# Performance work log

Hardware: AMD Instinct MI355X
Metric: run time of the kernel (lower is better)

The kernel has to match this reference:

```python
import jax, jax.numpy as jnp
import numpy as np

HIDDEN = 768
FFN = 3072
E = 8
TOP_K = 2


def setup_inputs() -> dict:
    key = jax.random.key(0)
    k_x, k_r, k_w1, k_w2 = jax.random.split(key, 4)
    x = jax.random.normal(k_x, (1, 1024, HIDDEN), dtype=jnp.float32)
    # nn.Linear(hidden, E, bias=False): weight applied as x @ W^T; store as [H, E]
    bound = 1.0 / np.sqrt(HIDDEN)
    router_w = jax.random.uniform(k_r, (HIDDEN, E), minval=-bound, maxval=bound, dtype=jnp.float32)
    w1 = jax.random.normal(k_w1, (E, HIDDEN, FFN), dtype=jnp.float32) * 0.02
    w2 = jax.random.normal(k_w2, (E, FFN, HIDDEN), dtype=jnp.float32) * 0.02
    return {"x": x, "router_w": router_w, "w1": w1, "w2": w2}


def reference(x, router_w, w1, w2):
    B, T, H = x.shape
    xf = x.reshape(-1, H)                                  # [N, H]
    logits = xf @ router_w                                 # [N, E] (eval mode: no noise)
    probs = jax.nn.softmax(logits, axis=-1)
    top_v, top_i = jax.lax.top_k(probs, TOP_K)             # [N, K]
    top_v = top_v / jnp.sum(top_v, axis=-1, keepdims=True)  # renormalize top-k probs
    # Combine top-k weights into a dense per-expert gate; zero gates make the
    # dense per-expert computation mathematically identical to sparse dispatch.
    gates = jnp.sum(jax.nn.one_hot(top_i, E, dtype=xf.dtype) * top_v[..., None], axis=1)  # [N, E]
    h = jax.nn.gelu(jnp.einsum('nh,ehf->enf', xf, w1), approximate=False)  # [E, N, F]
    y = jnp.einsum('enf,efh->enh', h, w2)                  # [E, N, H]
    out = jnp.einsum('ne,enh->nh', gates, y)               # [N, H]
    return out.reshape(B, T, H)
```

## Files before the change

kernel.cpp:

```cpp
#include <hip/hip_runtime.h>
#include <cmath>

#define NTOK 1024
#define HD   768
#define FF   3072
#define NE   8
#define NSLOT (NTOK * 2)
#define BK   64

#define NB_ROUTER 256
#define NB_CONV   4608
#define NB_FFN1   1152
#define KSPLIT    4
#define KSEG      (FF / KSPLIT)
#define NB_FFN2   (24 * 6 * KSPLIT)

typedef unsigned short u16;
typedef unsigned int   u32;
typedef __bf16 bf16x8 __attribute__((ext_vector_type(8)));
typedef float  f32x4  __attribute__((ext_vector_type(4)));
typedef u16    u16x8  __attribute__((ext_vector_type(8)));

__device__ __forceinline__ u16 f2bf(float f) {
  union { float f; u32 u; } v; v.f = f;
  u32 r = v.u + 0x7FFFu + ((v.u >> 16) & 1u);
  return (u16)(r >> 16);
}

__device__ __forceinline__ void load16(const void* g, void* l) {
  __builtin_amdgcn_global_load_lds(
      (const __attribute__((address_space(1))) u32*)g,
      (__attribute__((address_space(3))) u32*)l, 16, 0, 0);
}

__device__ __forceinline__ void conv_tile_dma(
    const float* __restrict__ src, u16* __restrict__ dst,
    int K, int N, int k0, int n0, float* lt, int tid, int lane, int wid)
{
  const int kr = wid * 16;
#pragma unroll
  for (int j = 0; j < 4; ++j) {
    const int k  = kr + j * 4 + (lane >> 4);
    const int sc = ((lane & 15) * 4) ^ (((k >> 3) & 3) << 3);
    load16(src + (size_t)(k0 + k) * N + n0 + sc,
           lt + (size_t)(kr + j * 4) * 64);
  }
  __syncthreads();
#pragma unroll
  for (int h = 0; h < 2; ++h) {
    const int c  = tid + h * 256;
    const int n  = c >> 3;
    const int ko = c & 7;
    const int sx = (ko & 3) << 3;
    u16x8 vv;
#pragma unroll
    for (int d = 0; d < 8; ++d)
      vv[d] = f2bf(lt[(ko * 8 + d) * 64 + (n ^ sx)]);
    *(u16x8*)(dst + (size_t)(n0 + n) * K + k0 + ko * 8) = vv;
  }
}

__global__ __launch_bounds__(256) void conv1_router_kernel(
    const float* __restrict__ w1, u16* __restrict__ w1t,
    const float* __restrict__ x, const float* __restrict__ rw,
    u16* __restrict__ xb, int* __restrict__ ti, float* __restrict__ tg,
    int* __restrict__ tos, float* __restrict__ gos, int* __restrict__ seg,
    int* __restrict__ done, float* __restrict__ out)
{
  __shared__ __align__(16) float lt[64 * 64];
  __shared__ int soff[NE], scnt[NE], spos[NE], lastFlag;
  const int tid  = threadIdx.x;
  const int lane = tid & 63;
  const int wid  = tid >> 6;

  if (blockIdx.x >= NB_ROUTER) {
    const int cid = blockIdx.x - NB_ROUTER;
    const int z   = cid / 576;
    const int rem = cid % 576;
    conv_tile_dma(w1 + (size_t)z * HD * FF, w1t + (size_t)z * FF * HD,
                  HD, FF, (rem / 48) * 64, (rem % 48) * 64, lt, tid, lane, wid);
    return;
  }

  {
    float4* o4 = (float4*)out;
    const float4 zz = {0.f, 0.f, 0.f, 0.f};
#pragma unroll
    for (int i = 0; i < 3; ++i) o4[(size_t)blockIdx.x * 768 + i * 256 + tid] = zz;
  }

  const int t = blockIdx.x * 4 + wid;
  const float* xrow = x + (size_t)t * HD;
  u16* xbrow = xb + (size_t)t * HD;

  float acc[NE] = {};
#pragma unroll
  for (int j = 0; j < 12; ++j) {
    const int h = lane + j * 64;
    const float xv = xrow[h];
    xbrow[h] = f2bf(xv);
    const float4 r0 = *(const float4*)(rw + h * 8);
    const float4 r1 = *(const float4*)(rw + h * 8 + 4);
    acc[0] += xv * r0.x; acc[1] += xv * r0.y;
    acc[2] += xv * r0.z; acc[3] += xv * r0.w;
    acc[4] += xv * r1.x; acc[5] += xv * r1.y;
    acc[6] += xv * r1.z; acc[7] += xv * r1.w;
  }
#pragma unroll
  for (int e = 0; e < NE; ++e) {
    float v = acc[e];
#pragma unroll
    for (int off = 32; off; off >>= 1) v += __shfl_down(v, off, 64);
    acc[e] = v;
  }
  if (lane == 0) {
    float v0 = -1e30f, v1 = -1e30f; int i0 = 0, i1 = 0;
#pragma unroll
    for (int e = 0; e < NE; ++e) {
      const float p = acc[e];
      if (p > v0) { v1 = v0; i1 = i0; v0 = p; i0 = e; }
      else if (p > v1) { v1 = p; i1 = e; }
    }
    const float e1 = expf(v1 - v0);
    ti[2 * t] = i0;      ti[2 * t + 1] = i1;
    tg[2 * t] = 1.0f / (1.0f + e1);
    tg[2 * t + 1] = e1 / (1.0f + e1);
  }

  __syncthreads();
  __threadfence();
  if (tid == 0) lastFlag = (atomicAdd(done, 1) == NB_ROUTER - 1);
  __syncthreads();
  if (!lastFlag) return;
  __threadfence();

  if (tid < NE) scnt[tid] = 0;
  __syncthreads();
  int   mye[8]; float myg[8];
#pragma unroll
  for (int j = 0; j < 8; ++j) {
    const int s = tid * 8 + j;
    mye[j] = ti[s]; myg[j] = tg[s];
    atomicAdd(&scnt[mye[j]], 1);
  }
  __syncthreads();
  if (tid == 0) {
    int o = 0;
    for (int e = 0; e < NE; ++e) {
      soff[e] = o; seg[e] = o; seg[NE + e] = scnt[e]; o += scnt[e];
    }
  }
  if (tid < NE) spos[tid] = 0;
  __syncthreads();
#pragma unroll
  for (int j = 0; j < 8; ++j) {
    const int s = tid * 8 + j;
    const int p = atomicAdd(&spos[mye[j]], 1);
    const int o = soff[mye[j]] + p;
    tos[o] = s >> 1;
    gos[o] = myg[j];
  }
}

__device__ __forceinline__ int find_expert(const int* __restrict__ seg,
                                           int mt, int* m0_out) {
  int e = -1, m0 = 0, off = 0;
#pragma unroll
  for (int ee = 0; ee < NE; ++ee) {
    const int T = (seg[NE + ee] + 127) >> 7;
    if (e < 0 && mt < off + T) { e = ee; m0 = (mt - off) << 7; }
    off += T;
  }
  *m0_out = m0;
  return e;
}

__global__ __launch_bounds__(256) void ffn1_conv2_kernel(
    const u16* __restrict__ xb, const u16* __restrict__ w1t,
    const int* __restrict__ tos, const int* __restrict__ seg,
    u16* __restrict__ hbuf,
    const float* __restrict__ w2, u16* __restrict__ w2t)
{
  __shared__ __align__(16) char smem[25088];
  const int tid  = threadIdx.x;
  const int lane = tid & 63;
  const int wid  = tid >> 6;

  const int g  = blockIdx.x / 5;
  const int r5 = blockIdx.x % 5;

  if (r5) {
    const int cid = g * 4 + (r5 - 1);
    const int z   = cid / 576;
    const int rem = cid % 576;
    conv_tile_dma(w2 + (size_t)z * FF * HD, w2t + (size_t)z * HD * FF,
                  FF, HD, (rem % 48) * 64, (rem / 48) * 64,
                  (float*)smem, tid, lane, wid);
    return;
  }

  const int mt = g / 48, nt = g % 48;
  int m0;
  const int e = find_expert(seg, mt, &m0);
  if (e < 0) return;
  const int cnt   = seg[NE + e];
  const int start = seg[e];
  const int n0    = nt * 64;

  u16* As   = (u16*)smem;
  u16* Bs   = (u16*)(smem + 16384);
  int* toks = (int*)(smem + 24576);

  if (tid < 128) toks[tid] = tos[start + min(m0 + tid, cnt - 1)];
  __syncthreads();

  const int rsub = lane >> 3;
  const int c8   = (lane & 7) ^ rsub;

  const u16* ag[4]; u16* al[4];
#pragma unroll
  for (int i = 0; i < 4; ++i) {
    const int rb = wid * 8 + i * 32;
    ag[i] = xb + (size_t)toks[rb + rsub] * HD + c8 * 8;
    al[i] = As + rb * 64;
  }
  const u16* bg[2]; u16* bl[2];
#pragma unroll
  for (int i = 0; i < 2; ++i) {
    const int rb = wid * 8 + i * 32;
    bg[i] = w1t + ((size_t)e * FF + n0 + rb + rsub) * HD + c8 * 8;
    bl[i] = Bs + rb * 64;
  }

  const int wm  = (wid >> 1) << 6;
  const int wn  = (wid & 1) << 5;
  const int q   = lane >> 4;
  const int r16 = lane & 15;

  f32x4 acc[4][2] = {};

  for (int k0 = 0; k0 < HD; k0 += BK) {
#pragma unroll
    for (int i = 0; i < 4; ++i) load16(ag[i] + k0, al[i]);
#pragma unroll
    for (int i = 0; i < 2; ++i) load16(bg[i] + k0, bl[i]);
    __syncthreads();
#pragma unroll
    for (int s = 0; s < 2; ++s) {
      const int pa = ((s << 2) + q) ^ (r16 & 7);
      bf16x8 af[4], bf[2];
#pragma unroll
      for (int t = 0; t < 4; ++t)
        af[t] = *(const bf16x8*)(&As[(wm + t * 16 + r16) * 64 + pa * 8]);
#pragma unroll
      for (int t = 0; t < 2; ++t)
        bf[t] = *(const bf16x8*)(&Bs[(wn + t * 16 + r16) * 64 + pa * 8]);
#pragma unroll
      for (int t = 0; t < 4; ++t)
#pragma unroll
        for (int c = 0; c < 2; ++c)
          acc[t][c] = __builtin_amdgcn_mfma_f32_16x16x32_bf16(af[t], bf[c], acc[t][c], 0, 0, 0);
    }
    __syncthreads();
  }

#pragma unroll
  for (int t = 0; t < 4; ++t) {
    const int mbase = m0 + wm + t * 16 + q * 4;
#pragma unroll
    for (int i = 0; i < 4; ++i) {
      if (mbase + i < cnt) {
        u16* drow = hbuf + (size_t)(start + mbase + i) * FF + n0 + wn;
#pragma unroll
        for (int c = 0; c < 2; ++c) {
          float v = acc[t][c][i];
          v = 0.5f * v * (1.0f + erff(v * 0.70710678118f));
          drow[c * 16 + r16] = f2bf(v);
        }
      }
    }
  }
}

__global__ __launch_bounds__(256) void ffn2_kernel(
    const u16* __restrict__ hbuf, const u16* __restrict__ w2t,
    const int* __restrict__ tos, const float* __restrict__ gos,
    const int* __restrict__ seg, float* __restrict__ out)
{
  const int fid  = blockIdx.x;
  const int mt   = fid / 24;
  const int rest = fid % 24;
  const int n0   = (rest >> 2) << 7;
  const int ks   = rest & 3;
  int m0;
  const int e = find_expert(seg, mt, &m0);
  if (e < 0) return;
  const int cnt   = seg[NE + e];
  const int start = seg[e];
  const int kbase = ks * KSEG;

  __shared__ __align__(16) u16 As[128 * 64];
  __shared__ __align__(16) u16 Bs[128 * 64];
  __shared__ int   toks[128];
  __shared__ float gates[128];

  const int tid = threadIdx.x;
  if (tid < 128) {
    const int idx = start + min(m0 + tid, cnt - 1);
    toks[tid]  = tos[idx];
    gates[tid] = gos[idx];
  }
  __syncthreads();

  const int lane = tid & 63;
  const int wid  = tid >> 6;
  const int rsub = lane >> 3;
  const int c8   = (lane & 7) ^ rsub;

  const u16* ag[4]; u16* al[4];
#pragma unroll
  for (int i = 0; i < 4; ++i) {
    const int rb = wid * 8 + i * 32;
    ag[i] = hbuf + (size_t)(start + min(m0 + rb + rsub, cnt - 1)) * FF + kbase + c8 * 8;
    al[i] = As + rb * 64;
  }
  const u16* bg[4]; u16* bl[4];
#pragma unroll
  for (int i = 0; i < 4; ++i) {
    const int rb = wid * 8 + i * 32;
    bg[i] = w2t + ((size_t)e * HD + n0 + rb + rsub) * FF + kbase + c8 * 8;
    bl[i] = Bs + rb * 64;
  }

  const int wm  = (wid >> 1) << 6;
  const int wn  = (wid & 1) << 6;
  const int q   = lane >> 4;
  const int r16 = lane & 15;

  f32x4 acc[4][4] = {};

  for (int k0 = 0; k0 < KSEG; k0 += BK) {
#pragma unroll
    for (int i = 0; i < 4; ++i) load16(ag[i] + k0, al[i]);
#pragma unroll
    for (int i = 0; i < 4; ++i) load16(bg[i] + k0, bl[i]);
    __syncthreads();
#pragma unroll
    for (int s = 0; s < 2; ++s) {
      const int pa = ((s << 2) + q) ^ (r16 & 7);
      bf16x8 af[4], bf[4];
#pragma unroll
      for (int t = 0; t < 4; ++t)
        af[t] = *(const bf16x8*)(&As[(wm + t * 16 + r16) * 64 + pa * 8]);
#pragma unroll
      for (int c = 0; c < 4; ++c)
        bf[c] = *(const bf16x8*)(&Bs[(wn + c * 16 + r16) * 64 + pa * 8]);
#pragma unroll
      for (int t = 0; t < 4; ++t)
#pragma unroll
        for (int c = 0; c < 4; ++c)
          acc[t][c] = __builtin_amdgcn_mfma_f32_16x16x32_bf16(af[t], bf[c], acc[t][c], 0, 0, 0);
    }
    __syncthreads();
  }

#pragma unroll
  for (int t = 0; t < 4; ++t) {
    const int mbase = wm + t * 16 + q * 4;
#pragma unroll
    for (int i = 0; i < 4; ++i) {
      const int mloc = mbase + i;
      if (m0 + mloc < cnt) {
        const int tok  = toks[mloc];
        const float gv = gates[mloc];
        float* drow = out + (size_t)tok * HD + n0 + wn;
#pragma unroll
        for (int c = 0; c < 4; ++c)
          atomicAdd(drow + c * 16 + r16, gv * acc[t][c][i]);
      }
    }
  }
}

extern "C" void kernel_launch(void* const* d_in, const int* in_sizes, int n_in,
                              void* d_out, int out_size, void* d_ws, size_t ws_size,
                              hipStream_t stream) {
  const float* x  = (const float*)d_in[0];
  const float* rw = (const float*)d_in[1];
  const float* w1 = (const float*)d_in[2];
  const float* w2 = (const float*)d_in[3];
  float* out = (float*)d_out;

  char* ws = (char*)d_ws;
  const size_t o_xb    = 0;
  const size_t o_hbuf  = o_xb + (size_t)NTOK * HD * 2;
  const size_t o_tos   = o_hbuf + (size_t)NSLOT * FF * 2;
  const size_t o_gos   = o_tos + (size_t)NSLOT * 4;
  const size_t o_seg   = o_gos + (size_t)NSLOT * 4;
  const size_t o_done  = o_seg + 64 * 4;
  const size_t o_ti    = o_done + 64;
  const size_t o_tg    = o_ti + (size_t)NSLOT * 4;
  const size_t o_w1t   = (o_tg + (size_t)NSLOT * 4 + 255) & ~(size_t)255;
  const size_t o_w2t   = o_w1t + (size_t)NE * HD * FF * 2;
  u16*   xb    = (u16*)(ws + o_xb);
  u16*   hbuf  = (u16*)(ws + o_hbuf);
  int*   tos   = (int*)(ws + o_tos);
  float* gos   = (float*)(ws + o_gos);
  int*   seg   = (int*)(ws + o_seg);
  int*   done  = (int*)(ws + o_done);
  int*   ti    = (int*)(ws + o_ti);
  float* tg    = (float*)(ws + o_tg);
  u16*   w1t   = (u16*)(ws + o_w1t);
  u16*   w2t   = (u16*)(ws + o_w2t);

  hipMemsetAsync(done, 0, 64, stream);
  hipLaunchKernelGGL(conv1_router_kernel, dim3(NB_ROUTER + NB_CONV), dim3(256), 0, stream,
                     w1, w1t, x, rw, xb, ti, tg, tos, gos, seg, done, out);
  hipLaunchKernelGGL(ffn1_conv2_kernel, dim3(NB_FFN1 * 5), dim3(256), 0, stream,
                     xb, w1t, tos, seg, hbuf, w2, w2t);
  hipLaunchKernelGGL(ffn2_kernel, dim3(NB_FFN2), dim3(256), 0, stream,
                     hbuf, w2t, tos, gos, seg, out);
}
```

Baseline: 273.6 us.

## Fuse MoE pipeline into one persistent kernel with grid barriers

Replaces the three launches (router+w1 conversion, ffn1+w2 conversion, ffn2) with a single 1024-block persistent kernel that separates phases with atomic grid barriers. The weight transpose-convert tiles change to 128x64 tiles that use register loads and a padded LDS transpose instead of LDS DMA. ffn2 tiles are narrowed to 64 columns to produce more work units. The aim is to remove launch gaps and tail effects between stages. It relies on all 1024 blocks being co-resident for the spin barriers, and risks deadlock or stalls if occupancy is insufficient.

```diff
diff --git a/kernel.cpp b/kernel.cpp
--- a/kernel.cpp
+++ b/kernel.cpp
@@ -7,13 +7,20 @@
 #define NE   8
 #define NSLOT (NTOK * 2)
 #define BK   64
-
+#define CLD  130
+
+#define NBLK      1024
 #define NB_ROUTER 256
-#define NB_CONV   4608
-#define NB_FFN1   1152
+
+#define NT_CONV   2304
+#define NU_FFN1   1152
+#define NU_P1     (NU_FFN1 + NT_CONV)
 #define KSPLIT    4
 #define KSEG      (FF / KSPLIT)
-#define NB_FFN2   (24 * 6 * KSPLIT)
+#define NU_FFN2   (24 * 12 * KSPLIT)
+
+#define TGT1 (NBLK + 1)
+#define TGT2 (TGT1 + NBLK)
 
 typedef unsigned short u16;
 typedef unsigned int   u32;
@@ -33,132 +40,36 @@
       (__attribute__((address_space(3))) u32*)l, 16, 0, 0);
 }
 
-__device__ __forceinline__ void conv_tile_dma(
+__device__ __forceinline__ void conv_tile(
     const float* __restrict__ src, u16* __restrict__ dst,
-    int K, int N, int k0, int n0, float* lt, int tid, int lane, int wid)
+    int K, int N, int k0, int n0, u16* lt, int tid, int lane, int wid)
 {
-  const int kr = wid * 16;
-#pragma unroll
-  for (int j = 0; j < 4; ++j) {
-    const int k  = kr + j * 4 + (lane >> 4);
-    const int sc = ((lane & 15) * 4) ^ (((k >> 3) & 3) << 3);
-    load16(src + (size_t)(k0 + k) * N + n0 + sc,
-           lt + (size_t)(kr + j * 4) * 64);
+  const int rr = tid >> 4;
+  const int cc = (tid & 15) << 2;
+
+  const float* s0 = src + (size_t)(k0 + rr) * N + n0 + cc;
+  float4 v[8];
+#pragma unroll
+  for (int j = 0; j < 8; ++j) v[j] = *(const float4*)(s0 + (size_t)j * 16 * N);
+  __builtin_amdgcn_sched_barrier(0);
+
+#pragma unroll
+  for (int j = 0; j < 8; ++j) {
+    const int k = j * 16 + rr;
+    lt[(cc + 0) * CLD + k] = f2bf(v[j].x); lt[(cc + 1) * CLD + k] = f2bf(v[j].y);
+    lt[(cc + 2) * CLD + k] = f2bf(v[j].z); lt[(cc + 3) * CLD + k] = f2bf(v[j].w);
   }
   __syncthreads();
-#pragma unroll
-  for (int h = 0; h < 2; ++h) {
-    const int c  = tid + h * 256;
-    const int n  = c >> 3;
-    const int ko = c & 7;
-    const int sx = (ko & 3) << 3;
+
+  const int l15 = lane & 15;
+  const int r4  = lane >> 4;
+#pragma unroll
+  for (int s = 0; s < 4; ++s) {
+    const int r = wid * 16 + s * 4 + r4;
     u16x8 vv;
 #pragma unroll
-    for (int d = 0; d < 8; ++d)
-      vv[d] = f2bf(lt[(ko * 8 + d) * 64 + (n ^ sx)]);
-    *(u16x8*)(dst + (size_t)(n0 + n) * K + k0 + ko * 8) = vv;
-  }
-}
-
-__global__ __launch_bounds__(256) void conv1_router_kernel(
-    const float* __restrict__ w1, u16* __restrict__ w1t,
-    const float* __restrict__ x, const float* __restrict__ rw,
-    u16* __restrict__ xb, int* __restrict__ ti, float* __restrict__ tg,
-    int* __restrict__ tos, float* __restrict__ gos, int* __restrict__ seg,
-    int* __restrict__ done, float* __restrict__ out)
-{
-  __shared__ __align__(16) float lt[64 * 64];
-  __shared__ int soff[NE], scnt[NE], spos[NE], lastFlag;
-  const int tid  = threadIdx.x;
-  const int lane = tid & 63;
-  const int wid  = tid >> 6;
-
-  if (blockIdx.x >= NB_ROUTER) {
-    const int cid = blockIdx.x - NB_ROUTER;
-    const int z   = cid / 576;
-    const int rem = cid % 576;
-    conv_tile_dma(w1 + (size_t)z * HD * FF, w1t + (size_t)z * FF * HD,
-                  HD, FF, (rem / 48) * 64, (rem % 48) * 64, lt, tid, lane, wid);
-    return;
-  }
-
-  {
-    float4* o4 = (float4*)out;
-    const float4 zz = {0.f, 0.f, 0.f, 0.f};
-#pragma unroll
-    for (int i = 0; i < 3; ++i) o4[(size_t)blockIdx.x * 768 + i * 256 + tid] = zz;
-  }
-
-  const int t = blockIdx.x * 4 + wid;
-  const float* xrow = x + (size_t)t * HD;
-  u16* xbrow = xb + (size_t)t * HD;
-
-  float acc[NE] = {};
-#pragma unroll
-  for (int j = 0; j < 12; ++j) {
-    const int h = lane + j * 64;
-    const float xv = xrow[h];
-    xbrow[h] = f2bf(xv);
-    const float4 r0 = *(const float4*)(rw + h * 8);
-    const float4 r1 = *(const float4*)(rw + h * 8 + 4);
-    acc[0] += xv * r0.x; acc[1] += xv * r0.y;
-    acc[2] += xv * r0.z; acc[3] += xv * r0.w;
-    acc[4] += xv * r1.x; acc[5] += xv * r1.y;
-    acc[6] += xv * r1.z; acc[7] += xv * r1.w;
-  }
-#pragma unroll
-  for (int e = 0; e < NE; ++e) {
-    float v = acc[e];
-#pragma unroll
-    for (int off = 32; off; off >>= 1) v += __shfl_down(v, off, 64);
-    acc[e] = v;
-  }
-  if (lane == 0) {
-    float v0 = -1e30f, v1 = -1e30f; int i0 = 0, i1 = 0;
-#pragma unroll
-    for (int e = 0; e < NE; ++e) {
-      const float p = acc[e];
-      if (p > v0) { v1 = v0; i1 = i0; v0 = p; i0 = e; }
-      else if (p > v1) { v1 = p; i1 = e; }
-    }
-    const float e1 = expf(v1 - v0);
-    ti[2 * t] = i0;      ti[2 * t + 1] = i1;
-    tg[2 * t] = 1.0f / (1.0f + e1);
-    tg[2 * t + 1] = e1 / (1.0f + e1);
-  }
-
-  __syncthreads();
-  __threadfence();
-  if (tid == 0) lastFlag = (atomicAdd(done, 1) == NB_ROUTER - 1);
-  __syncthreads();
-  if (!lastFlag) return;
-  __threadfence();
-
-  if (tid < NE) scnt[tid] = 0;
-  __syncthreads();
-  int   mye[8]; float myg[8];
-#pragma unroll
-  for (int j = 0; j < 8; ++j) {
-    const int s = tid * 8 + j;
-    mye[j] = ti[s]; myg[j] = tg[s];
-    atomicAdd(&scnt[mye[j]], 1);
-  }
-  __syncthreads();
-  if (tid == 0) {
-    int o = 0;
-    for (int e = 0; e < NE; ++e) {
-      soff[e] = o; seg[e] = o; seg[NE + e] = scnt[e]; o += scnt[e];
-    }
-  }
-  if (tid < NE) spos[tid] = 0;
-  __syncthreads();
-#pragma unroll
-  for (int j = 0; j < 8; ++j) {
-    const int s = tid * 8 + j;
-    const int p = atomicAdd(&spos[mye[j]], 1);
-    const int o = soff[mye[j]] + p;
-    tos[o] = s >> 1;
-    gos[o] = myg[j];
+    for (int d = 0; d < 8; ++d) vv[d] = lt[r * CLD + l15 * 8 + d];
+    *(u16x8*)(dst + (size_t)(n0 + r) * K + k0 + l15 * 8) = vv;
   }
 }
 
@@ -175,31 +86,12 @@
   return e;
 }
 
-__global__ __launch_bounds__(256) void ffn1_conv2_kernel(
-    const u16* __restrict__ xb, const u16* __restrict__ w1t,
+__device__ __forceinline__ void ffn1_unit(
+    int fid, const u16* __restrict__ xb, const u16* __restrict__ w1t,
     const int* __restrict__ tos, const int* __restrict__ seg,
-    u16* __restrict__ hbuf,
-    const float* __restrict__ w2, u16* __restrict__ w2t)
+    u16* __restrict__ hbuf, char* smem, int tid, int lane, int wid)
 {
-  __shared__ __align__(16) char smem[25088];
-  const int tid  = threadIdx.x;
-  const int lane = tid & 63;
-  const int wid  = tid >> 6;
-
-  const int g  = blockIdx.x / 5;
-  const int r5 = blockIdx.x % 5;
-
-  if (r5) {
-    const int cid = g * 4 + (r5 - 1);
-    const int z   = cid / 576;
-    const int rem = cid % 576;
-    conv_tile_dma(w2 + (size_t)z * FF * HD, w2t + (size_t)z * HD * FF,
-                  FF, HD, (rem % 48) * 64, (rem / 48) * 64,
-                  (float*)smem, tid, lane, wid);
-    return;
-  }
-
-  const int mt = g / 48, nt = g % 48;
+  const int mt = fid / 48, nt = fid % 48;
   int m0;
   const int e = find_expert(seg, mt, &m0);
   if (e < 0) return;
@@ -273,24 +165,24 @@
         u16* drow = hbuf + (size_t)(start + mbase + i) * FF + n0 + wn;
 #pragma unroll
         for (int c = 0; c < 2; ++c) {
-          float v = acc[t][c][i];
-          v = 0.5f * v * (1.0f + erff(v * 0.70710678118f));
-          drow[c * 16 + r16] = f2bf(v);
+          float vv = acc[t][c][i];
+          vv = 0.5f * vv * (1.0f + erff(vv * 0.70710678118f));
+          drow[c * 16 + r16] = f2bf(vv);
         }
       }
     }
   }
 }
 
-__global__ __launch_bounds__(256) void ffn2_kernel(
-    const u16* __restrict__ hbuf, const u16* __restrict__ w2t,
+__device__ __forceinline__ void ffn2_unit(
+    int u, const u16* __restrict__ hbuf, const u16* __restrict__ w2t,
     const int* __restrict__ tos, const float* __restrict__ gos,
-    const int* __restrict__ seg, float* __restrict__ out)
+    const int* __restrict__ seg, float* __restrict__ out,
+    char* smem, int tid, int lane, int wid)
 {
-  const int fid  = blockIdx.x;
-  const int mt   = fid / 24;
-  const int rest = fid % 24;
-  const int n0   = (rest >> 2) << 7;
+  const int mt   = u / 48;
+  const int rest = u % 48;
+  const int n0   = (rest >> 2) * 64;
   const int ks   = rest & 3;
   int m0;
   const int e = find_expert(seg, mt, &m0);
@@ -299,12 +191,11 @@
   const int start = seg[e];
   const int kbase = ks * KSEG;
 
-  __shared__ __align__(16) u16 As[128 * 64];
-  __shared__ __align__(16) u16 Bs[128 * 64];
-  __shared__ int   toks[128];
-  __shared__ float gates[128];
-
-  const int tid = threadIdx.x;
+  u16*   As    = (u16*)smem;
+  u16*   Bs    = (u16*)(smem + 16384);
+  int*   toks  = (int*)(smem + 24576);
+  float* gates = (float*)(smem + 25088);
+
   if (tid < 128) {
     const int idx = start + min(m0 + tid, cnt - 1);
     toks[tid]  = tos[idx];
@@ -312,8 +203,6 @@
   }
   __syncthreads();
 
-  const int lane = tid & 63;
-  const int wid  = tid >> 6;
   const int rsub = lane >> 3;
   const int c8   = (lane & 7) ^ rsub;
 
@@ -324,41 +213,41 @@
     ag[i] = hbuf + (size_t)(start + min(m0 + rb + rsub, cnt - 1)) * FF + kbase + c8 * 8;
     al[i] = As + rb * 64;
   }
-  const u16* bg[4]; u16* bl[4];
-#pragma unroll
-  for (int i = 0; i < 4; ++i) {
+  const u16* bg[2]; u16* bl[2];
+#pragma unroll
+  for (int i = 0; i < 2; ++i) {
     const int rb = wid * 8 + i * 32;
     bg[i] = w2t + ((size_t)e * HD + n0 + rb + rsub) * FF + kbase + c8 * 8;
     bl[i] = Bs + rb * 64;
   }
 
   const int wm  = (wid >> 1) << 6;
-  const int wn  = (wid & 1) << 6;
+  const int wn  = (wid & 1) << 5;
   const int q   = lane >> 4;
   const int r16 = lane & 15;
 
-  f32x4 acc[4][4] = {};
+  f32x4 acc[4][2] = {};
 
   for (int k0 = 0; k0 < KSEG; k0 += BK) {
 #pragma unroll
     for (int i = 0; i < 4; ++i) load16(ag[i] + k0, al[i]);
 #pragma unroll
-    for (int i = 0; i < 4; ++i) load16(bg[i] + k0, bl[i]);
+    for (int i = 0; i < 2; ++i) load16(bg[i] + k0, bl[i]);
     __syncthreads();
 #pragma unroll
     for (int s = 0; s < 2; ++s) {
       const int pa = ((s << 2) + q) ^ (r16 & 7);
-      bf16x8 af[4], bf[4];
+      bf16x8 af[4], bf[2];
 #pragma unroll
       for (int t = 0; t < 4; ++t)
         af[t] = *(const bf16x8*)(&As[(wm + t * 16 + r16) * 64 + pa * 8]);
 #pragma unroll
-      for (int c = 0; c < 4; ++c)
-        bf[c] = *(const bf16x8*)(&Bs[(wn + c * 16 + r16) * 64 + pa * 8]);
+      for (int t = 0; t < 2; ++t)
+        bf[t] = *(const bf16x8*)(&Bs[(wn + t * 16 + r16) * 64 + pa * 8]);
 #pragma unroll
       for (int t = 0; t < 4; ++t)
 #pragma unroll
-        for (int c = 0; c < 4; ++c)
+        for (int c = 0; c < 2; ++c)
           acc[t][c] = __builtin_amdgcn_mfma_f32_16x16x32_bf16(af[t], bf[c], acc[t][c], 0, 0, 0);
     }
     __syncthreads();
@@ -375,10 +264,174 @@
         const float gv = gates[mloc];
         float* drow = out + (size_t)tok * HD + n0 + wn;
 #pragma unroll
-        for (int c = 0; c < 4; ++c)
+        for (int c = 0; c < 2; ++c)
           atomicAdd(drow + c * 16 + r16, gv * acc[t][c][i]);
       }
     }
+  }
+}
+
+__device__ __forceinline__ void grid_bar(int* bar, int target) {
+  __syncthreads();
+  if (threadIdx.x == 0) {
+    __threadfence();
+    __hip_atomic_fetch_add(bar, 1, __ATOMIC_RELEASE, __HIP_MEMORY_SCOPE_AGENT);
+    while (__hip_atomic_load(bar, __ATOMIC_ACQUIRE, __HIP_MEMORY_SCOPE_AGENT) < target)
+      __builtin_amdgcn_s_sleep(2);
+  }
+  __syncthreads();
+  __threadfence();
+}
+
+__global__ __launch_bounds__(256, 4) void moe_persistent(
+    const float* __restrict__ w1, const float* __restrict__ w2,
+    u16* __restrict__ w1t, u16* __restrict__ w2t,
+    const float* __restrict__ x, const float* __restrict__ rw,
+    u16* __restrict__ xb, int* __restrict__ ti, float* __restrict__ tg,
+    int* __restrict__ tos, float* __restrict__ gos, int* __restrict__ seg,
+    int* __restrict__ ctr, u16* __restrict__ hbuf, float* __restrict__ out)
+{
+  __shared__ __align__(16) char smem[25600];
+  __shared__ int soff[NE], scnt[NE], spos[NE], lastFlag;
+  const int tid  = threadIdx.x;
+  const int lane = tid & 63;
+  const int wid  = tid >> 6;
+  const int bid  = blockIdx.x;
+  int* bar = &ctr[0];
+
+  {
+    float4* o4 = (float4*)out;
+    const float4 zz = {0.f, 0.f, 0.f, 0.f};
+    if (tid < 192) o4[(size_t)bid * 192 + tid] = zz;
+  }
+
+  if (bid < NB_ROUTER) {
+    const int t = bid * 4 + wid;
+    const float* xrow = x + (size_t)t * HD;
+    u16* xbrow = xb + (size_t)t * HD;
+
+    float acc[NE] = {};
+#pragma unroll
+    for (int j = 0; j < 12; ++j) {
+      const int h = lane + j * 64;
+      const float xv = xrow[h];
+      xbrow[h] = f2bf(xv);
+      const float4 r0 = *(const float4*)(rw + h * 8);
+      const float4 r1 = *(const float4*)(rw + h * 8 + 4);
+      acc[0] += xv * r0.x; acc[1] += xv * r0.y;
+      acc[2] += xv * r0.z; acc[3] += xv * r0.w;
+      acc[4] += xv * r1.x; acc[5] += xv * r1.y;
+      acc[6] += xv * r1.z; acc[7] += xv * r1.w;
+    }
+#pragma unroll
+    for (int e = 0; e < NE; ++e) {
+      float v = acc[e];
+#pragma unroll
+      for (int off = 32; off; off >>= 1) v += __shfl_down(v, off, 64);
+      acc[e] = v;
+    }
+    if (lane == 0) {
+      float v0 = -1e30f, v1 = -1e30f; int i0 = 0, i1 = 0;
+#pragma unroll
+      for (int e = 0; e < NE; ++e) {
+        const float p = acc[e];
+        if (p > v0) { v1 = v0; i1 = i0; v0 = p; i0 = e; }
+        else if (p > v1) { v1 = p; i1 = e; }
+      }
+      const float e1 = expf(v1 - v0);
+      ti[2 * t] = i0;      ti[2 * t + 1] = i1;
+      tg[2 * t] = 1.0f / (1.0f + e1);
+      tg[2 * t + 1] = e1 / (1.0f + e1);
+    }
+
+    __syncthreads();
+    __threadfence();
+    if (tid == 0) lastFlag = (atomicAdd(&ctr[1], 1) == NB_ROUTER - 1);
+    __syncthreads();
+    if (lastFlag) {
+      __threadfence();
+      if (tid < NE) scnt[tid] = 0;
+      __syncthreads();
+      int mye[8]; float myg[8];
+#pragma unroll
+      for (int j = 0; j < 8; ++j) {
+        const int s = tid * 8 + j;
+        mye[j] = ti[s]; myg[j] = tg[s];
+        atomicAdd(&scnt[mye[j]], 1);
+      }
+      __syncthreads();
+      if (tid == 0) {
+        int o = 0;
+        for (int e = 0; e < NE; ++e) {
+          soff[e] = o; seg[e] = o; seg[NE + e] = scnt[e]; o += scnt[e];
+        }
+      }
+      if (tid < NE) spos[tid] = 0;
+      __syncthreads();
+#pragma unroll
+      for (int j = 0; j < 8; ++j) {
+        const int s = tid * 8 + j;
+        const int p = atomicAdd(&spos[mye[j]], 1);
+        const int o = soff[mye[j]] + p;
+        tos[o] = s >> 1;
+        gos[o] = myg[j];
+      }
+      __syncthreads();
+      __threadfence();
+      if (tid == 0)
+        __hip_atomic_fetch_add(bar, 1, __ATOMIC_RELEASE, __HIP_MEMORY_SCOPE_AGENT);
+    }
+  }
+
+  {
+    u16* lt = (u16*)smem;
+    {
+      const int cid = bid;
+      __syncthreads();
+      conv_tile(w1 + (size_t)(cid / 288) * HD * FF,
+                w1t + (size_t)(cid / 288) * FF * HD, HD, FF,
+                ((cid % 288) / 48) * 128, ((cid % 288) % 48) * 64,
+                lt, tid, lane, wid);
+    }
+    {
+      const int cid = bid + 1024;
+      __syncthreads();
+      conv_tile(w1 + (size_t)(cid / 288) * HD * FF,
+                w1t + (size_t)(cid / 288) * FF * HD, HD, FF,
+                ((cid % 288) / 48) * 128, ((cid % 288) % 48) * 64,
+                lt, tid, lane, wid);
+    }
+    if (bid >= 768) {
+      const int cid = 2048 + (bid - 768);
+      __syncthreads();
+      conv_tile(w1 + (size_t)(cid / 288) * HD * FF,
+                w1t + (size_t)(cid / 288) * FF * HD, HD, FF,
+                ((cid % 288) / 48) * 128, ((cid % 288) % 48) * 64,
+                lt, tid, lane, wid);
+    }
+  }
+
+  grid_bar(bar, TGT1);
+
+  for (int u = bid; u < NU_P1; u += NBLK) {
+    __syncthreads();
+    if (u % 3 == 0) {
+      ffn1_unit(u / 3, xb, w1t, tos, seg, hbuf, smem, tid, lane, wid);
+    } else {
+      const int cid = u - u / 3 - 1;
+      const int z   = cid / 288;
+      const int rem = cid % 288;
+      conv_tile(w2 + (size_t)z * FF * HD, w2t + (size_t)z * HD * FF,
+                FF, HD, (rem % 24) * 128, (rem / 24) * 64,
+                (u16*)smem, tid, lane, wid);
+    }
+  }
+
+  grid_bar(bar, TGT2);
+
+  for (int u = bid; u < NU_FFN2; u += NBLK) {
+    __syncthreads();
+    ffn2_unit(u, hbuf, w2t, tos, gos, seg, out, smem, tid, lane, wid);
   }
 }
 
@@ -397,8 +450,8 @@
   const size_t o_tos   = o_hbuf + (size_t)NSLOT * FF * 2;
   const size_t o_gos   = o_tos + (size_t)NSLOT * 4;
   const size_t o_seg   = o_gos + (size_t)NSLOT * 4;
-  const size_t o_done  = o_seg + 64 * 4;
-  const size_t o_ti    = o_done + 64;
+  const size_t o_ctr   = o_seg + 64 * 4;
+  const size_t o_ti    = o_ctr + 64;
   const size_t o_tg    = o_ti + (size_t)NSLOT * 4;
   const size_t o_w1t   = (o_tg + (size_t)NSLOT * 4 + 255) & ~(size_t)255;
   const size_t o_w2t   = o_w1t + (size_t)NE * HD * FF * 2;
@@ -407,17 +460,14 @@
   int*   tos   = (int*)(ws + o_tos);
   float* gos   = (float*)(ws + o_gos);
   int*   seg   = (int*)(ws + o_seg);
-  int*   done  = (int*)(ws + o_done);
+  int*   ctr   = (int*)(ws + o_ctr);
   int*   ti    = (int*)(ws + o_ti);
   float* tg    = (float*)(ws + o_tg);
   u16*   w1t   = (u16*)(ws + o_w1t);
   u16*   w2t   = (u16*)(ws + o_w2t);
 
-  hipMemsetAsync(done, 0, 64, stream);
-  hipLaunchKernelGGL(conv1_router_kernel, dim3(NB_ROUTER + NB_CONV), dim3(256), 0, stream,
-                     w1, w1t, x, rw, xb, ti, tg, tos, gos, seg, done, out);
-  hipLaunchKernelGGL(ffn1_conv2_kernel, dim3(NB_FFN1 * 5), dim3(256), 0, stream,
-                     xb, w1t, tos, seg, hbuf, w2, w2t);
-  hipLaunchKernelGGL(ffn2_kernel, dim3(NB_FFN2), dim3(256), 0, stream,
-                     hbuf, w2t, tos, gos, seg, out);
-}
+  hipMemsetAsync(ctr, 0, 64, stream);
+  hipLaunchKernelGGL(moe_persistent, dim3(NBLK), dim3(256), 0, stream,
+                     w1, w2, w1t, w2t, x, rw, xb, ti, tg, tos, gos, seg,
+                     ctr, hbuf, out);
+}
```

New measurement: 798.2 us. +191.7%, slower.

## Drop separate weight transpose passes; convert fp32 weights to bf16 inside GEMM tiles

Applied to the files above, without the earlier changes.

The separate w1/w2 fp32-to-bf16 transpose tiles that wrote full bf16 copies of both weight tensors are removed. Both FFN GEMMs now read the fp32 weights directly in their natural [K,N] layout into registers, convert to bf16 and write swizzled LDS tiles, double-buffering the global loads one k-step ahead. FFN2 shrinks its N tile from 128 to 64 to fit the register-staged path, so it launches more blocks. This saves a full write and re-read of the converted weights, but every tile re-reads fp32 weights (twice the bytes of bf16) and repeats the conversion work, since several M tiles per expert share each weight tile.

```diff
diff --git a/kernel.cpp b/kernel.cpp
--- a/kernel.cpp
+++ b/kernel.cpp
@@ -9,11 +9,10 @@
 #define BK   64
 
 #define NB_ROUTER 256
-#define NB_CONV   4608
-#define NB_FFN1   1152
+#define NU_FFN1   1152
 #define KSPLIT    4
 #define KSEG      (FF / KSPLIT)
-#define NB_FFN2   (24 * 6 * KSPLIT)
+#define NU_FFN2   1152
 
 typedef unsigned short u16;
 typedef unsigned int   u32;
@@ -33,63 +32,39 @@
       (__attribute__((address_space(3))) u32*)l, 16, 0, 0);
 }
 
-__device__ __forceinline__ void conv_tile_dma(
-    const float* __restrict__ src, u16* __restrict__ dst,
-    int K, int N, int k0, int n0, float* lt, int tid, int lane, int wid)
-{
-  const int kr = wid * 16;
-#pragma unroll
-  for (int j = 0; j < 4; ++j) {
-    const int k  = kr + j * 4 + (lane >> 4);
-    const int sc = ((lane & 15) * 4) ^ (((k >> 3) & 3) << 3);
-    load16(src + (size_t)(k0 + k) * N + n0 + sc,
-           lt + (size_t)(kr + j * 4) * 64);
-  }
-  __syncthreads();
-#pragma unroll
-  for (int h = 0; h < 2; ++h) {
-    const int c  = tid + h * 256;
-    const int n  = c >> 3;
-    const int ko = c & 7;
-    const int sx = (ko & 3) << 3;
-    u16x8 vv;
-#pragma unroll
-    for (int d = 0; d < 8; ++d)
-      vv[d] = f2bf(lt[(ko * 8 + d) * 64 + (n ^ sx)]);
-    *(u16x8*)(dst + (size_t)(n0 + n) * K + k0 + ko * 8) = vv;
-  }
-}
-
-__global__ __launch_bounds__(256) void conv1_router_kernel(
-    const float* __restrict__ w1, u16* __restrict__ w1t,
+__device__ __forceinline__ int find_expert(const int* __restrict__ seg,
+                                           int mt, int* m0_out) {
+  int e = -1, m0 = 0, off = 0;
+#pragma unroll
+  for (int ee = 0; ee < NE; ++ee) {
+    const int T = (seg[NE + ee] + 127) >> 7;
+    if (e < 0 && mt < off + T) { e = ee; m0 = (mt - off) << 7; }
+    off += T;
+  }
+  *m0_out = m0;
+  return e;
+}
+
+__global__ __launch_bounds__(256) void router_kernel(
     const float* __restrict__ x, const float* __restrict__ rw,
     u16* __restrict__ xb, int* __restrict__ ti, float* __restrict__ tg,
     int* __restrict__ tos, float* __restrict__ gos, int* __restrict__ seg,
-    int* __restrict__ done, float* __restrict__ out)
+    int* __restrict__ ctr, float* __restrict__ out)
 {
-  __shared__ __align__(16) float lt[64 * 64];
   __shared__ int soff[NE], scnt[NE], spos[NE], lastFlag;
   const int tid  = threadIdx.x;
   const int lane = tid & 63;
   const int wid  = tid >> 6;
-
-  if (blockIdx.x >= NB_ROUTER) {
-    const int cid = blockIdx.x - NB_ROUTER;
-    const int z   = cid / 576;
-    const int rem = cid % 576;
-    conv_tile_dma(w1 + (size_t)z * HD * FF, w1t + (size_t)z * FF * HD,
-                  HD, FF, (rem / 48) * 64, (rem % 48) * 64, lt, tid, lane, wid);
-    return;
-  }
+  const int bid  = blockIdx.x;
 
   {
     float4* o4 = (float4*)out;
     const float4 zz = {0.f, 0.f, 0.f, 0.f};
 #pragma unroll
-    for (int i = 0; i < 3; ++i) o4[(size_t)blockIdx.x * 768 + i * 256 + tid] = zz;
-  }
-
-  const int t = blockIdx.x * 4 + wid;
+    for (int i = 0; i < 3; ++i) o4[(size_t)bid * 768 + i * 256 + tid] = zz;
+  }
+
+  const int t = bid * 4 + wid;
   const float* xrow = x + (size_t)t * HD;
   u16* xbrow = xb + (size_t)t * HD;
 
@@ -129,14 +104,14 @@
 
   __syncthreads();
   __threadfence();
-  if (tid == 0) lastFlag = (atomicAdd(done, 1) == NB_ROUTER - 1);
+  if (tid == 0) lastFlag = (atomicAdd(&ctr[1], 1) == NB_ROUTER - 1);
   __syncthreads();
   if (!lastFlag) return;
   __threadfence();
 
   if (tid < NE) scnt[tid] = 0;
   __syncthreads();
-  int   mye[8]; float myg[8];
+  int mye[8]; float myg[8];
 #pragma unroll
   for (int j = 0; j < 8; ++j) {
     const int s = tid * 8 + j;
@@ -149,6 +124,7 @@
     for (int e = 0; e < NE; ++e) {
       soff[e] = o; seg[e] = o; seg[NE + e] = scnt[e]; o += scnt[e];
     }
+    ctr[1] = 0;
   }
   if (tid < NE) spos[tid] = 0;
   __syncthreads();
@@ -162,58 +138,48 @@
   }
 }
 
-__device__ __forceinline__ int find_expert(const int* __restrict__ seg,
-                                           int mt, int* m0_out) {
-  int e = -1, m0 = 0, off = 0;
-#pragma unroll
-  for (int ee = 0; ee < NE; ++ee) {
-    const int T = (seg[NE + ee] + 127) >> 7;
-    if (e < 0 && mt < off + T) { e = ee; m0 = (mt - off) << 7; }
-    off += T;
-  }
-  *m0_out = m0;
-  return e;
-}
-
-__global__ __launch_bounds__(256) void ffn1_conv2_kernel(
-    const u16* __restrict__ xb, const u16* __restrict__ w1t,
+
+#define LOADB(BSRC, BN, K0, D) do {                                          \
+  _Pragma("unroll")                                                          \
+  for (int j = 0; j < 4; ++j)                                                \
+    D[j] = *(const f32x4*)((BSRC) + (size_t)((K0) + rr * 4 + j) * (BN));     \
+} while (0)
+
+#define WRITEB(D) do {                                                       \
+  _Pragma("unroll")                                                          \
+  for (int i = 0; i < 4; ++i) {                                              \
+    uint2 w;                                                                 \
+    w.x = (u32)f2bf(D[0][i]) | ((u32)f2bf(D[1][i]) << 16);                   \
+    w.y = (u32)f2bf(D[2][i]) | ((u32)f2bf(D[3][i]) << 16);                   \
+    *(uint2*)(&Bs[wofs[i]]) = w;                                             \
+  }                                                                          \
+} while (0)
+
+__global__ __launch_bounds__(256) void ffn1_kernel(
+    const u16* __restrict__ xb, const float* __restrict__ w1,
     const int* __restrict__ tos, const int* __restrict__ seg,
-    u16* __restrict__ hbuf,
-    const float* __restrict__ w2, u16* __restrict__ w2t)
+    u16* __restrict__ hbuf)
 {
-  __shared__ __align__(16) char smem[25088];
-  const int tid  = threadIdx.x;
-  const int lane = tid & 63;
-  const int wid  = tid >> 6;
-
-  const int g  = blockIdx.x / 5;
-  const int r5 = blockIdx.x % 5;
-
-  if (r5) {
-    const int cid = g * 4 + (r5 - 1);
-    const int z   = cid / 576;
-    const int rem = cid % 576;
-    conv_tile_dma(w2 + (size_t)z * FF * HD, w2t + (size_t)z * HD * FF,
-                  FF, HD, (rem % 48) * 64, (rem / 48) * 64,
-                  (float*)smem, tid, lane, wid);
-    return;
-  }
-
-  const int mt = g / 48, nt = g % 48;
+  const int fid = blockIdx.x;
+  const int mt = fid / 48, nt = fid % 48;
   int m0;
   const int e = find_expert(seg, mt, &m0);
   if (e < 0) return;
   const int cnt   = seg[NE + e];
   const int start = seg[e];
   const int n0    = nt * 64;
-
-  u16* As   = (u16*)smem;
-  u16* Bs   = (u16*)(smem + 16384);
-  int* toks = (int*)(smem + 24576);
-
+  const float* w1e = w1 + (size_t)e * HD * FF;
+
+  __shared__ __align__(16) u16 As[128 * 64];
+  __shared__ __align__(16) u16 Bs[64 * 64];
+  __shared__ int toks[128];
+
+  const int tid = threadIdx.x;
   if (tid < 128) toks[tid] = tos[start + min(m0 + tid, cnt - 1)];
   __syncthreads();
 
+  const int lane = tid & 63;
+  const int wid  = tid >> 6;
   const int rsub = lane >> 3;
   const int c8   = (lane & 7) ^ rsub;
 
@@ -224,12 +190,15 @@
     ag[i] = xb + (size_t)toks[rb + rsub] * HD + c8 * 8;
     al[i] = As + rb * 64;
   }
-  const u16* bg[2]; u16* bl[2];
-#pragma unroll
-  for (int i = 0; i < 2; ++i) {
-    const int rb = wid * 8 + i * 32;
-    bg[i] = w1t + ((size_t)e * FF + n0 + rb + rsub) * HD + c8 * 8;
-    bl[i] = Bs + rb * 64;
+
+  const int rr = tid >> 4;
+  const int cc = (tid & 15) << 2;
+  const float* bsrc = w1e + n0 + cc;
+  int wofs[4];
+#pragma unroll
+  for (int i = 0; i < 4; ++i) {
+    const int n = cc + i;
+    wofs[i] = n * 64 + (((rr >> 1) ^ (n & 7)) << 3) + ((rr & 1) << 2);
   }
 
   const int wm  = (wid >> 1) << 6;
@@ -238,13 +207,20 @@
   const int r16 = lane & 15;
 
   f32x4 acc[4][2] = {};
-
-  for (int k0 = 0; k0 < HD; k0 += BK) {
+  f32x4 breg[2][4];
+
+  LOADB(bsrc, FF, 0, breg[0]);
+#pragma unroll
+  for (int kk = 0; kk < 12; ++kk) {
+    const int k0 = kk * BK;
 #pragma unroll
     for (int i = 0; i < 4; ++i) load16(ag[i] + k0, al[i]);
-#pragma unroll
-    for (int i = 0; i < 2; ++i) load16(bg[i] + k0, bl[i]);
+    WRITEB(breg[kk & 1]);
     __syncthreads();
+    if (kk < 11) {
+      LOADB(bsrc, FF, k0 + BK, breg[(kk + 1) & 1]);
+      __builtin_amdgcn_sched_barrier(0);
+    }
 #pragma unroll
     for (int s = 0; s < 2; ++s) {
       const int pa = ((s << 2) + q) ^ (r16 & 7);
@@ -273,9 +249,9 @@
         u16* drow = hbuf + (size_t)(start + mbase + i) * FF + n0 + wn;
 #pragma unroll
         for (int c = 0; c < 2; ++c) {
-          float v = acc[t][c][i];
-          v = 0.5f * v * (1.0f + erff(v * 0.70710678118f));
-          drow[c * 16 + r16] = f2bf(v);
+          float vv = acc[t][c][i];
+          vv = 0.5f * vv * (1.0f + erff(vv * 0.70710678118f));
+          drow[c * 16 + r16] = f2bf(vv);
         }
       }
     }
@@ -283,14 +259,14 @@
 }
 
 __global__ __launch_bounds__(256) void ffn2_kernel(
-    const u16* __restrict__ hbuf, const u16* __restrict__ w2t,
+    const u16* __restrict__ hbuf, const float* __restrict__ w2,
     const int* __restrict__ tos, const float* __restrict__ gos,
     const int* __restrict__ seg, float* __restrict__ out)
 {
-  const int fid  = blockIdx.x;
-  const int mt   = fid / 24;
-  const int rest = fid % 24;
-  const int n0   = (rest >> 2) << 7;
+  const int u    = blockIdx.x;
+  const int mt   = u / 48;
+  const int rest = u % 48;
+  const int n0   = (rest >> 2) * 64;
   const int ks   = rest & 3;
   int m0;
   const int e = find_expert(seg, mt, &m0);
@@ -298,9 +274,10 @@
   const int cnt   = seg[NE + e];
   const int start = seg[e];
   const int kbase = ks * KSEG;
+  const float* w2e = w2 + (size_t)e * FF * HD;
 
   __shared__ __align__(16) u16 As[128 * 64];
-  __shared__ __align__(16) u16 Bs[128 * 64];
+  __shared__ __align__(16) u16 Bs[64 * 64];
   __shared__ int   toks[128];
   __shared__ float gates[128];
 
@@ -324,41 +301,51 @@
     ag[i] = hbuf + (size_t)(start + min(m0 + rb + rsub, cnt - 1)) * FF + kbase + c8 * 8;
     al[i] = As + rb * 64;
   }
-  const u16* bg[4]; u16* bl[4];
+
+  const int rr = tid >> 4;
+  const int cc = (tid & 15) << 2;
+  const float* bsrc = w2e + (size_t)kbase * HD + n0 + cc;
+  int wofs[4];
 #pragma unroll
   for (int i = 0; i < 4; ++i) {
-    const int rb = wid * 8 + i * 32;
-    bg[i] = w2t + ((size_t)e * HD + n0 + rb + rsub) * FF + kbase + c8 * 8;
-    bl[i] = Bs + rb * 64;
+    const int n = cc + i;
+    wofs[i] = n * 64 + (((rr >> 1) ^ (n & 7)) << 3) + ((rr & 1) << 2);
   }
 
   const int wm  = (wid >> 1) << 6;
-  const int wn  = (wid & 1) << 6;
+  const int wn  = (wid & 1) << 5;
   const int q   = lane >> 4;
   const int r16 = lane & 15;
 
-  f32x4 acc[4][4] = {};
-
-  for (int k0 = 0; k0 < KSEG; k0 += BK) {
+  f32x4 acc[4][2] = {};
+  f32x4 breg[2][4];
+
+  LOADB(bsrc, HD, 0, breg[0]);
+#pragma unroll
+  for (int kk = 0; kk < 12; ++kk) {
+    const int k0 = kk * BK;
 #pragma unroll
     for (int i = 0; i < 4; ++i) load16(ag[i] + k0, al[i]);
-#pragma unroll
-    for (int i = 0; i < 4; ++i) load16(bg[i] + k0, bl[i]);
+    WRITEB(breg[kk & 1]);
     __syncthreads();
+    if (kk < 11) {
+      LOADB(bsrc, HD, k0 + BK, breg[(kk + 1) & 1]);
+      __builtin_amdgcn_sched_barrier(0);
+    }
 #pragma unroll
     for (int s = 0; s < 2; ++s) {
       const int pa = ((s << 2) + q) ^ (r16 & 7);
-      bf16x8 af[4], bf[4];
+      bf16x8 af[4], bf[2];
 #pragma unroll
       for (int t = 0; t < 4; ++t)
         af[t] = *(const bf16x8*)(&As[(wm + t * 16 + r16) * 64 + pa * 8]);
 #pragma unroll
-      for (int c = 0; c < 4; ++c)
-        bf[c] = *(const bf16x8*)(&Bs[(wn + c * 16 + r16) * 64 + pa * 8]);
+      for (int t = 0; t < 2; ++t)
+        bf[t] = *(const bf16x8*)(&Bs[(wn + t * 16 + r16) * 64 + pa * 8]);
 #pragma unroll
       for (int t = 0; t < 4; ++t)
 #pragma unroll
-        for (int c = 0; c < 4; ++c)
+        for (int c = 0; c < 2; ++c)
           acc[t][c] = __builtin_amdgcn_mfma_f32_16x16x32_bf16(af[t], bf[c], acc[t][c], 0, 0, 0);
     }
     __syncthreads();
@@ -375,7 +362,7 @@
         const float gv = gates[mloc];
         float* drow = out + (size_t)tok * HD + n0 + wn;
 #pragma unroll
-        for (int c = 0; c < 4; ++c)
+        for (int c = 0; c < 2; ++c)
           atomicAdd(drow + c * 16 + r16, gv * acc[t][c][i]);
       }
     }
@@ -397,27 +384,23 @@
   const size_t o_tos   = o_hbuf + (size_t)NSLOT * FF * 2;
   const size_t o_gos   = o_tos + (size_t)NSLOT * 4;
   const size_t o_seg   = o_gos + (size_t)NSLOT * 4;
-  const size_t o_done  = o_seg + 64 * 4;
-  const size_t o_ti    = o_done + 64;
+  const size_t o_ctr   = o_seg + 64 * 4;
+  const size_t o_ti    = o_ctr + 64;
   const size_t o_tg    = o_ti + (size_t)NSLOT * 4;
-  const size_t o_w1t   = (o_tg + (size_t)NSLOT * 4 + 255) & ~(size_t)255;
-  const size_t o_w2t   = o_w1t + (size_t)NE * HD * FF * 2;
   u16*   xb    = (u16*)(ws + o_xb);
   u16*   hbuf  = (u16*)(ws + o_hbuf);
   int*   tos   = (int*)(ws + o_tos);
   float* gos   = (float*)(ws + o_gos);
   int*   seg   = (int*)(ws + o_seg);
-  int*   done  = (int*)(ws + o_done);
+  int*   ctr   = (int*)(ws + o_ctr);
   int*   ti    = (int*)(ws + o_ti);
   float* tg    = (float*)(ws + o_tg);
-  u16*   w1t   = (u16*)(ws + o_w1t);
-  u16*   w2t   = (u16*)(ws + o_w2t);
-
-  hipMemsetAsync(done, 0, 64, stream);
-  hipLaunchKernelGGL(conv1_router_kernel, dim3(NB_ROUTER + NB_CONV), dim3(256), 0, stream,
-                     w1, w1t, x, rw, xb, ti, tg, tos, gos, seg, done, out);
-  hipLaunchKernelGGL(ffn1_conv2_kernel, dim3(NB_FFN1 * 5), dim3(256), 0, stream,
-                     xb, w1t, tos, seg, hbuf, w2, w2t);
-  hipLaunchKernelGGL(ffn2_kernel, dim3(NB_FFN2), dim3(256), 0, stream,
-                     hbuf, w2t, tos, gos, seg, out);
-}
+
+  hipMemsetAsync(ctr, 0, 64, stream);
+  hipLaunchKernelGGL(router_kernel, dim3(NB_ROUTER), dim3(256), 0, stream,
+                     x, rw, xb, ti, tg, tos, gos, seg, ctr, out);
+  hipLaunchKernelGGL(ffn1_kernel, dim3(NU_FFN1), dim3(256), 0, stream,
+                     xb, w1, tos, seg, hbuf);
+  hipLaunchKernelGGL(ffn2_kernel, dim3(NU_FFN2), dim3(256), 0, stream,
+                     hbuf, w2, tos, gos, seg, out);
+}
```

After: 266.0 us. 2.8% less time.
